# Kernel tuning notes

Measured on AMD Instinct MI355X. Metric: run time of the kernel, lower is better.

Reference implementation:

```python
import jax, jax.numpy as jnp
import numpy as np

ALPHA = 0.3      # keras LeakyReLU default
BN_EPS = 1e-3    # keras BatchNormalization default
RF, STRIDE = 8, 8


def leaky(x):
    return jnp.where(x >= 0, x, ALPHA * x)


def batchnorm(x, gamma, beta):
    # training-mode BN (train_flag=True): batch statistics over N,H,W
    mean = jnp.mean(x, axis=(0, 1, 2), keepdims=True)
    var = jnp.var(x, axis=(0, 1, 2), keepdims=True)
    return gamma * (x - mean) * jax.lax.rsqrt(var + BN_EPS) + beta


def cbl(x, W, gamma, beta):
    y = jax.lax.conv_general_dilated(x, W, (1, 1), 'SAME',
                                     dimension_numbers=('NHWC', 'HWIO', 'NHWC'))
    return leaky(batchnorm(y, gamma, beta))


def tcbl(x, W, gamma, beta):
    y = jax.lax.conv_transpose(x, W, (2, 2), 'SAME',
                               dimension_numbers=('NHWC', 'HWIO', 'NHWC'))
    return leaky(batchnorm(y, gamma, beta))


def setup_inputs() -> dict:
    key = jax.random.key(0)
    ks = jax.random.split(key, 8)
    B, H, W, C = 8, 128, 128, 128
    nH = (H - RF) // STRIDE + 1
    nW = (W - RF) // STRIDE + 1
    nWin = nH * nW  # 256
    inputs = jax.random.normal(ks[0], (B, H, W, C), dtype=jnp.float32)
    conv_scale = 1.0 / np.sqrt(3 * 3 * C)
    Wq = jax.random.normal(ks[1], (3, 3, C, 128), dtype=jnp.float32) * conv_scale
    Wk = jax.random.normal(ks[2], (3, 3, C, 128), dtype=jnp.float32) * conv_scale
    beta_bias = jax.random.normal(ks[3], (1, 1, 1, nWin), dtype=jnp.float32) * 0.05
    Wt = jax.random.normal(ks[4], (4, 4, nWin, 128), dtype=jnp.float32) / np.sqrt(4 * 4 * nWin)
    return {
        'inputs': inputs,
        'Wq': Wq, 'gq': jnp.ones((128,), jnp.float32), 'bq': jnp.zeros((128,), jnp.float32),
        'Wk': Wk, 'gk': jnp.ones((128,), jnp.float32), 'bk': jnp.zeros((128,), jnp.float32),
        'beta_bias': beta_bias,
        'g1': jnp.ones((nWin,), jnp.float32), 'b1': jnp.zeros((nWin,), jnp.float32),
        'Wt': Wt, 'gt': jnp.ones((128,), jnp.float32), 'bt': jnp.zeros((128,), jnp.float32),
    }


def reference(inputs, Wq, gq, bq, Wk, gk, bk, beta_bias, g1, b1, Wt, gt, bt):
    Q = cbl(inputs, Wq, gq, bq)   # (B,H,W,C)
    K = cbl(inputs, Wk, gk, bk)
    B, H, W, C = Q.shape
    nH = (H - RF) // STRIDE + 1
    nW = (W - RF) // STRIDE + 1
    # window start indices -> (n, RF) gather index grids
    hh = (jnp.arange(nH) * STRIDE)[:, None] + jnp.arange(RF)[None, :]
    ww = (jnp.arange(nW) * STRIDE)[:, None] + jnp.arange(RF)[None, :]

    def patches(x):
        # (B, nH, nW, RF, RF, C) -> (B, nWin, RF*RF*C)
        p = x[:, hh[:, None, :, None], ww[None, :, None, :], :]
        return p.reshape(B, nH * nW, RF * RF * C)

    Qp = patches(Q)
    Kp = patches(K)
    # sim[b, f, q] = <K window f, Q window q>; collapses the 4-nested loop
    sim = jnp.einsum('bfd,bqd->bfq', Kp, Qp).reshape(B, nH, nW, nH * nW)
    sim = sim + beta_bias
    act = leaky(batchnorm(sim, g1, b1))
    return tcbl(act, Wt, gt, bt)  # (B, 2*nH, 2*nW, 128)
```

## Files before the change

### kernel.cpp

```cpp
#include <hip/hip_runtime.h>

typedef __attribute__((ext_vector_type(8))) short bf16x8;
typedef __attribute__((ext_vector_type(8))) unsigned short u16x8;
typedef __attribute__((ext_vector_type(4))) float f32x4;

__device__ __forceinline__ unsigned short f2b(float x) {
    unsigned int u = __float_as_uint(x);
    u += 0x7FFFu + ((u >> 16) & 1u);
    return (unsigned short)(u >> 16);
}
__device__ __forceinline__ float b2f(unsigned short h) {
    return __uint_as_float(((unsigned int)h) << 16);
}
__device__ __forceinline__ float lrelu(float v) { return v >= 0.f ? v : 0.3f * v; }

#define GLL(gp, lp) __builtin_amdgcn_global_load_lds( \
    (const __attribute__((address_space(1))) unsigned int*)(gp), \
    (__attribute__((address_space(3))) unsigned int*)(lp), 16, 0, 0)


__global__ __launch_bounds__(256) void k0a_prep(
        const float* __restrict__ Wq, const float* __restrict__ Wk,
        const float* __restrict__ Wt, unsigned short* __restrict__ WqT,
        unsigned short* __restrict__ WkT, unsigned short* __restrict__ WtT,
        float* __restrict__ S) {
    int idx = blockIdx.x * 256 + threadIdx.x;
    int gs = gridDim.x * 256;
    for (int i = idx; i < 2048; i += gs) S[i] = 0.f;
    for (int i = idx; i < 147456; i += gs) {
        int tap = i >> 14, r = i & 16383, ci = r >> 7, co = r & 127;
        int ch = ci >> 6, e = ci & 63;
        int dst = ((tap * 2 + ch) * 128 + co) * 64 + (((e >> 3) ^ (co & 7)) << 3) + (e & 7);
        WqT[dst] = f2b(Wq[i]);
        WkT[dst] = f2b(Wk[i]);
    }
    for (int i = idx; i < 524288; i += gs) {
        int t = i >> 15, r = i & 32767, ci = r >> 7, co = r & 127;
        WtT[(((size_t)t << 7) + co) * 256 + ci] = f2b(Wt[i]);
    }
}

__global__ __launch_bounds__(256) void k0b_padx(const float* __restrict__ X,
                                                unsigned short* __restrict__ Xb) {
    int c = blockIdx.x * 256 + threadIdx.x;
    int k8 = c & 7;
    int t = c >> 3;
    int wp = t % 130; t /= 130;
    int ch = t & 1; t >>= 1;
    int hp = t % 130; int b = t / 130;
    u16x8 o;
    if (hp >= 1 && hp <= 128 && wp >= 1 && wp <= 128) {
        const float* s = X + (((size_t)(b * 128 + hp - 1) * 128) + (wp - 1)) * 128 + ch * 64 + k8 * 8;
        float4 f0 = *(const float4*)(s);
        float4 f1 = *(const float4*)(s + 4);
        o[0] = f2b(f0.x); o[1] = f2b(f0.y); o[2] = f2b(f0.z); o[3] = f2b(f0.w);
        o[4] = f2b(f1.x); o[5] = f2b(f1.y); o[6] = f2b(f1.z); o[7] = f2b(f1.w);
    } else {
#pragma unroll
        for (int j = 0; j < 8; ++j) o[j] = 0;
    }
    *(u16x8*)&Xb[(size_t)c * 8] = o;
}

__global__ __launch_bounds__(512, 4) void k1_conv(
        const unsigned short* __restrict__ Xb,
        const unsigned short* __restrict__ WqT, const unsigned short* __restrict__ WkT,
        unsigned short* __restrict__ Qraw, unsigned short* __restrict__ Kraw,
        float* __restrict__ S) {
    __shared__ unsigned short s_row[2 * 130 * 72];
    __shared__ unsigned short s_w[2][128 * 64];
    __shared__ float s_st[256];
    const int tid = threadIdx.x;
    const int x = blockIdx.x;
    const int conv = x & 1, hp = (x >> 1) & 63, b = x >> 7;
    const int h0 = hp * 2;
    const int lane = tid & 63, wv = tid >> 6;
    const int wm = wv & 3, wn = wv >> 2;
    const int l15 = lane & 15, kof = (lane >> 4) * 8;
    const int ar = wm >> 1;
    const int awb = (wm & 1) * 64;
    const int nb = wn * 64;

    const unsigned short* W = conv ? WkT : WqT;
    const int gofs = wv * 2048 + lane * 16;

    f32x4 acc[4][4];
#pragma unroll
    for (int i = 0; i < 4; ++i)
#pragma unroll
        for (int j = 0; j < 4; ++j) acc[i][j] = (f32x4){0.f, 0.f, 0.f, 0.f};
    if (tid < 256) s_st[tid] = 0.f;

    {
        const char* src = (const char*)W;
        char* dst = (char*)&s_w[0][0] + wv * 2048;
        GLL(src + gofs, dst);
        GLL(src + gofs + 1024, dst + 1024);
    }

#pragma unroll
    for (int ch = 0; ch < 2; ++ch) {
#pragma unroll
        for (int dy = 0; dy < 3; ++dy) {
#pragma unroll
            for (int dx = 0; dx < 3; ++dx) {
                const int p = (ch * 3 + dy) * 3 + dx;
                __builtin_amdgcn_s_barrier();
                if (dx == 0) {
                    const unsigned short* src0 = Xb + (size_t)((b * 130 + h0 + dy) * 2 + ch) * 8320;
                    const unsigned short* src1 = Xb + (size_t)((b * 130 + h0 + dy + 1) * 2 + ch) * 8320;
                    for (int c = tid; c < 2080; c += 512) {
                        int r = (c >= 1040);
                        int cw = r ? c - 1040 : c;
                        int w = cw >> 3, k8 = cw & 7;
                        *(u16x8*)&s_row[(r * 130 + w) * 72 + k8 * 8] =
                            *(const u16x8*)&((r ? src1 : src0)[cw * 8]);
                    }
                }
                if (p < 17) {
                    const int pn = p + 1;
                    const int nch = pn / 9, ntap = pn % 9;
                    const char* src = (const char*)(W + ((size_t)(ntap * 2 + nch) << 13));
                    char* dst = (char*)&s_w[pn & 1][0] + wv * 2048;
                    GLL(src + gofs, dst);
                    GLL(src + gofs + 1024, dst + 1024);
                    asm volatile("s_waitcnt vmcnt(2) lgkmcnt(0)" ::: "memory");
                } else {
                    asm volatile("s_waitcnt vmcnt(0) lgkmcnt(0)" ::: "memory");
                }
                __builtin_amdgcn_sched_barrier(0);
                __builtin_amdgcn_s_barrier();
                const unsigned short* wb = &s_w[p & 1][0];
#pragma unroll
                for (int kc = 0; kc < 2; ++kc) {
                    const int ci = kc * 32 + kof;
                    bf16x8 a[4], bb[4];
#pragma unroll
                    for (int mf = 0; mf < 4; ++mf)
                        a[mf] = *(const bf16x8*)&s_row[(ar * 130 + awb + mf * 16 + l15 + dx) * 72 + ci];
#pragma unroll
                    for (int nf = 0; nf < 4; ++nf) {
                        int co = nb + nf * 16 + l15;
                        bb[nf] = *(const bf16x8*)&wb[co * 64 + (((ci >> 3) ^ (co & 7)) << 3)];
                    }
#pragma unroll
                    for (int mf = 0; mf < 4; ++mf)
#pragma unroll
                        for (int nf = 0; nf < 4; ++nf)
                            acc[mf][nf] = __builtin_amdgcn_mfma_f32_16x16x32_bf16(
                                a[mf], bb[nf], acc[mf][nf], 0, 0, 0);
                }
            }
        }
    }
    __syncthreads();
    unsigned short* obase = conv ? Kraw : Qraw;
    const int h = h0 + ar;
    float sl[4] = {0.f, 0.f, 0.f, 0.f}, ssl[4] = {0.f, 0.f, 0.f, 0.f};
#pragma unroll
    for (int mf = 0; mf < 4; ++mf)
#pragma unroll
        for (int nf = 0; nf < 4; ++nf)
#pragma unroll
            for (int r = 0; r < 4; ++r) {
                float v = acc[mf][nf][r];
                int w = awb + mf * 16 + (lane >> 4) * 4 + r;
                int co = nb + nf * 16 + l15;
                obase[((size_t)(b * 128 + h) * 128 + w) * 128 + co] = f2b(v);
                sl[nf] += v; ssl[nf] += v * v;
            }
#pragma unroll
    for (int nf = 0; nf < 4; ++nf) {
        float s = sl[nf], ss = ssl[nf];
        s += __shfl_xor(s, 16); s += __shfl_xor(s, 32);
        ss += __shfl_xor(ss, 16); ss += __shfl_xor(ss, 32);
        if (lane < 16) {
            int chn = nb + nf * 16 + lane;
            atomicAdd(&s_st[chn], s);
            atomicAdd(&s_st[128 + chn], ss);
        }
    }
    __syncthreads();
    if (tid < 256) {
        int dst = (tid < 128) ? (conv * 128 + tid) : (256 + conv * 128 + (tid - 128));
        atomicAdd(&S[dst], s_st[tid]);
    }
}

__global__ void k2a_fin(const float* __restrict__ gq, const float* __restrict__ bq,
                        const float* __restrict__ gk, const float* __restrict__ bk,
                        const float* __restrict__ S, float* __restrict__ P) {
    int c = threadIdx.x;
    const float inv_n = 1.f / 131072.f;
    float mean = S[c] * inv_n;
    float var = S[256 + c] * inv_n - mean * mean;
    float g  = (c < 128) ? gq[c] : gk[c - 128];
    float be = (c < 128) ? bq[c] : bk[c - 128];
    float sc = g * rsqrtf(var + 1e-3f);
    P[c] = sc;
    P[256 + c] = be - mean * sc;
}

__global__ __launch_bounds__(512, 2) void k3_sim(const unsigned short* __restrict__ Qp,
                                                 const unsigned short* __restrict__ Kp,
                                                 const float* __restrict__ P,
                                                 float* __restrict__ part) {
    __shared__ unsigned short sA[128 * 136];
    __shared__ unsigned short sB[128 * 136];
    const int tid = threadIdx.x;
    const int x = blockIdx.x;
    const int kc = x & 15, ni = (x >> 4) & 1, mi = (x >> 5) & 1, b = x >> 6;
    const int lane = tid & 63, wv = tid >> 6;
    const int wm = wv & 1, wn = wv >> 1;
    f32x4 acc[4][2];
#pragma unroll
    for (int i = 0; i < 4; ++i)
#pragma unroll
        for (int j = 0; j < 2; ++j) acc[i][j] = (f32x4){0.f, 0.f, 0.f, 0.f};
    const int kof = (lane >> 4) * 8;
    const int arow = wm * 64 + (lane & 15);
    const int brow = wn * 32 + (lane & 15);

    for (int s = 0; s < 4; ++s) {
        const int p = kc * 4 + s, py = p >> 3, px = p & 7;
        __syncthreads();
        for (int c = tid; c < 2048; c += 512) {
            int r = c >> 4, k8 = c & 15;
            int cb = k8 * 8;
            int f = mi * 128 + r;
            size_t sa = ((size_t)(b * 128 + ((f >> 4) * 8 + py)) * 128 + ((f & 15) * 8 + px)) * 128 + cb;
            int q = ni * 128 + r;
            size_t sb = ((size_t)(b * 128 + ((q >> 4) * 8 + py)) * 128 + ((q & 15) * 8 + px)) * 128 + cb;
            u16x8 va = *(const u16x8*)&Kp[sa];
            u16x8 vb = *(const u16x8*)&Qp[sb];
            u16x8 oa, ob;
#pragma unroll
            for (int j = 0; j < 8; ++j) {
                float fk = b2f(va[j]);
                fk = lrelu(P[128 + cb + j] * fk + P[384 + cb + j]);
                oa[j] = f2b(fk);
                float fq = b2f(vb[j]);
                fq = lrelu(P[cb + j] * fq + P[256 + cb + j]);
                ob[j] = f2b(fq);
            }
            *(u16x8*)&sA[r * 136 + cb] = oa;
            *(u16x8*)&sB[r * 136 + cb] = ob;
        }
        __syncthreads();
#pragma unroll
        for (int k4 = 0; k4 < 4; ++k4) {
            const int ci = k4 * 32 + kof;
            bf16x8 a[4], bb[2];
#pragma unroll
            for (int mf = 0; mf < 4; ++mf)
                a[mf] = *(const bf16x8*)&sA[(arow + mf * 16) * 136 + ci];
#pragma unroll
            for (int nf = 0; nf < 2; ++nf)
                bb[nf] = *(const bf16x8*)&sB[(brow + nf * 16) * 136 + ci];
#pragma unroll
            for (int mf = 0; mf < 4; ++mf)
#pragma unroll
                for (int nf = 0; nf < 2; ++nf)
                    acc[mf][nf] = __builtin_amdgcn_mfma_f32_16x16x32_bf16(
                        a[mf], bb[nf], acc[mf][nf], 0, 0, 0);
        }
    }
    const size_t base = (size_t)(kc * 8 + b) * 65536;
#pragma unroll
    for (int mf = 0; mf < 4; ++mf)
#pragma unroll
        for (int nf = 0; nf < 2; ++nf)
#pragma unroll
            for (int r = 0; r < 4; ++r) {
                int f = mi * 128 + wm * 64 + mf * 16 + (lane >> 4) * 4 + r;
                int q = ni * 128 + wn * 32 + nf * 16 + (lane & 15);
                part[base + (size_t)f * 256 + q] = acc[mf][nf][r];
            }
}

__global__ __launch_bounds__(256) void k4_red(const float* __restrict__ part,
                                              const float* __restrict__ beta,
                                              float* __restrict__ sim, float* __restrict__ S) {
    int row0 = blockIdx.x * 8;
    int q = threadIdx.x;
    float bsum = 0.f, bss = 0.f;
    float bb = beta[q];
    for (int rr = 0; rr < 8; ++rr) {
        int row = row0 + rr;
        float s = 0.f;
#pragma unroll
        for (int kcc = 0; kcc < 16; ++kcc)
            s += part[(size_t)kcc * 524288 + (size_t)row * 256 + q];
        s += bb;
        sim[(size_t)row * 256 + q] = s;
        bsum += s; bss += s * s;
    }
    atomicAdd(&S[512 + q], bsum);
    atomicAdd(&S[768 + q], bss);
}

__global__ void k5a_fin(const float* __restrict__ g1, const float* __restrict__ b1,
                        const float* __restrict__ S, float* __restrict__ P) {
    int c = threadIdx.x;
    const float inv_n = 1.f / 2048.f;
    float mean = S[512 + c] * inv_n;
    float var = S[768 + c] * inv_n - mean * mean;
    float sc = g1[c] * rsqrtf(var + 1e-3f);
    P[512 + c] = sc;
    P[768 + c] = b1[c] - mean * sc;
}

__global__ __launch_bounds__(256) void k5b_act(const float* __restrict__ sim,
                                               const float* __restrict__ P,
                                               unsigned short* __restrict__ actp) {
    int c = blockIdx.x * 256 + threadIdx.x;
    int k8 = c & 31;
    int t = c >> 5;
    int jp = t % 18; t /= 18;
    int ip = t % 18; int b = t / 18;
    u16x8 o;
    if (ip >= 1 && ip <= 16 && jp >= 1 && jp <= 16) {
        int f = (ip - 1) * 16 + (jp - 1);
        const float* s = sim + (size_t)(b * 256 + f) * 256 + k8 * 8;
#pragma unroll
        for (int j = 0; j < 8; ++j) {
            int ci = k8 * 8 + j;
            o[j] = f2b(lrelu(P[512 + ci] * s[j] + P[768 + ci]));
        }
    } else {
#pragma unroll
        for (int j = 0; j < 8; ++j) o[j] = 0;
    }
    *(u16x8*)&actp[(size_t)c * 8] = o;
}

__global__ __launch_bounds__(512, 2) void k6_tconv(const unsigned short* __restrict__ actp,
                                                   const unsigned short* __restrict__ WtT,
                                                   float* __restrict__ y, float* __restrict__ S) {
    __shared__ unsigned short sA[64 * 264];
    __shared__ unsigned short sB[128 * 264];
    const int tid = threadIdx.x;
    const int x = blockIdx.x;
    const int iq = x & 3, pw = (x >> 2) & 1, ph = (x >> 3) & 1, b = x >> 4;
    const int lane = tid & 63, wv = tid >> 6;
    f32x4 acc[4];
#pragma unroll
    for (int i = 0; i < 4; ++i) acc[i] = (f32x4){0.f, 0.f, 0.f, 0.f};
    const int kof = (lane >> 4) * 8;
    const int arow = lane & 15;
    const int bco = wv * 16 + (lane & 15);

    for (int a2 = 0; a2 < 2; ++a2)
        for (int c2 = 0; c2 < 2; ++c2) {
            const int kh = ph + 2 * a2, kw = pw + 2 * c2;
            __syncthreads();
            for (int c = tid; c < 2048; c += 512) {
                int r = c >> 5, k8 = c & 31;
                int i = iq * 4 + (r >> 4), j = r & 15;
                size_t sa = (size_t)((b * 18 + (i + a2 + ph)) * 18 + (j + c2 + pw)) * 256 + k8 * 8;
                *(u16x8*)&sA[r * 264 + k8 * 8] = *(const u16x8*)&actp[sa];
            }
            for (int c = tid; c < 4096; c += 512) {
                int co = c >> 5, k8 = c & 31;
                size_t sb = (size_t)((kh * 4 + kw) * 128 + co) * 256 + k8 * 8;
                *(u16x8*)&sB[co * 264 + k8 * 8] = *(const u16x8*)&WtT[sb];
            }
            __syncthreads();
#pragma unroll
            for (int k8c = 0; k8c < 8; ++k8c) {
                const int ci = k8c * 32 + kof;
                bf16x8 bb = *(const bf16x8*)&sB[bco * 264 + ci];
#pragma unroll
                for (int mf = 0; mf < 4; ++mf) {
                    bf16x8 a = *(const bf16x8*)&sA[(arow + mf * 16) * 264 + ci];
                    acc[mf] = __builtin_amdgcn_mfma_f32_16x16x32_bf16(a, bb, acc[mf], 0, 0, 0);
                }
            }
        }
    float sl = 0.f, ssl = 0.f;
#pragma unroll
    for (int mf = 0; mf < 4; ++mf)
#pragma unroll
        for (int r = 0; r < 4; ++r) {
            float v = acc[mf][r];
            int m = mf * 16 + (lane >> 4) * 4 + r;
            int i = iq * 4 + (m >> 4), j = m & 15;
            int oh = 2 * i + ph, ow = 2 * j + pw;
            y[(size_t)((b * 32 + oh) * 32 + ow) * 128 + bco] = v;
            sl += v; ssl += v * v;
        }
    sl += __shfl_xor(sl, 16); sl += __shfl_xor(sl, 32);
    ssl += __shfl_xor(ssl, 16); ssl += __shfl_xor(ssl, 32);
    if (lane < 16) {
        atomicAdd(&S[1024 + wv * 16 + lane], sl);
        atomicAdd(&S[1152 + wv * 16 + lane], ssl);
    }
}

__global__ void k7_fin(const float* __restrict__ gt, const float* __restrict__ bt,
                       const float* __restrict__ S, float* __restrict__ P) {
    int c = threadIdx.x;
    const float inv_n = 1.f / 8192.f;
    float mean = S[1024 + c] * inv_n;
    float var = S[1152 + c] * inv_n - mean * mean;
    float sc = gt[c] * rsqrtf(var + 1e-3f);
    P[1024 + c] = sc;
    P[1280 + c] = bt[c] - mean * sc;
}

__global__ __launch_bounds__(256) void k8_out(const float* __restrict__ y,
                                              const float* __restrict__ P,
                                              float* __restrict__ out) {
    int c = blockIdx.x * 256 + threadIdx.x;
    const float4 v = *(const float4*)&y[(size_t)c * 4];
    int cb = (c & 31) * 4;
    float4 o;
    o.x = lrelu(P[1024 + cb + 0] * v.x + P[1280 + cb + 0]);
    o.y = lrelu(P[1024 + cb + 1] * v.y + P[1280 + cb + 1]);
    o.z = lrelu(P[1024 + cb + 2] * v.z + P[1280 + cb + 2]);
    o.w = lrelu(P[1024 + cb + 3] * v.w + P[1280 + cb + 3]);
    *(float4*)&out[(size_t)c * 4] = o;
}

extern "C" void kernel_launch(void* const* d_in, const int* in_sizes, int n_in,
                              void* d_out, int out_size, void* d_ws, size_t ws_size,
                              hipStream_t stream) {
    (void)in_sizes; (void)n_in; (void)out_size; (void)ws_size;
    const float* X    = (const float*)d_in[0];
    const float* Wq   = (const float*)d_in[1];
    const float* gq   = (const float*)d_in[2];
    const float* bq   = (const float*)d_in[3];
    const float* Wk   = (const float*)d_in[4];
    const float* gk   = (const float*)d_in[5];
    const float* bk   = (const float*)d_in[6];
    const float* beta = (const float*)d_in[7];
    const float* g1   = (const float*)d_in[8];
    const float* b1   = (const float*)d_in[9];
    const float* Wt   = (const float*)d_in[10];
    const float* gt   = (const float*)d_in[11];
    const float* bt   = (const float*)d_in[12];

    char* ws = (char*)d_ws;
    unsigned short* Qraw = (unsigned short*)(ws + 0ull);
    unsigned short* Kraw = (unsigned short*)(ws + 33554432ull);
    unsigned short* WqT  = (unsigned short*)(ws + 67108864ull);
    unsigned short* WkT  = (unsigned short*)(ws + 67403776ull);
    unsigned short* WtT  = (unsigned short*)(ws + 67698688ull);
    float* S             = (float*)(ws + 68747264ull);
    float* P             = (float*)(ws + 68755456ull);
    unsigned short* Xb   = (unsigned short*)(ws + 70858752ull);
    float* part          = (float*)(ws + 70858752ull);
    float* sim           = (float*)(ws + 0ull);
    unsigned short* actp = (unsigned short*)(ws + 4194304ull);
    float* y             = (float*)(ws + 8388608ull);
    float* out           = (float*)d_out;

    k0a_prep<<<1024, 256, 0, stream>>>(Wq, Wk, Wt, WqT, WkT, WtT, S);
    k0b_padx<<<8450, 256, 0, stream>>>(X, Xb);
    k1_conv<<<1024, 512, 0, stream>>>(Xb, WqT, WkT, Qraw, Kraw, S);
    k2a_fin<<<1, 256, 0, stream>>>(gq, bq, gk, bk, S, P);
    k3_sim<<<512, 512, 0, stream>>>(Qraw, Kraw, P, part);
    k4_red<<<256, 256, 0, stream>>>(part, beta, sim, S);
    k5a_fin<<<1, 256, 0, stream>>>(g1, b1, S, P);
    k5b_act<<<729, 256, 0, stream>>>(sim, P, actp);
    k6_tconv<<<128, 512, 0, stream>>>(actp, WtT, y, S);
    k7_fin<<<1, 128, 0, stream>>>(gt, bt, S, P);
    k8_out<<<1024, 256, 0, stream>>>(y, P, out);
}
```

Measured before the change: 178.5 us.

## Pipeline conv input rows via async LDS loads and fold BN finalize kernels into consumers

The padded input is relaid out as four 32-channel slabs with a lane-swizzled 136-wide row, so the conv kernel can stream input rows into double-buffered LDS with global_load_lds. Those row loads are prefetched one stage ahead alongside the weight tiles, instead of being copied synchronously through registers. The three single-block BN finalize kernels are removed and their scale/shift math is recomputed per block inside the consuming kernels, which cuts launches at the cost of redundant tiny work. MFMA sections are also wrapped in s_setprio.

```diff
diff --git a/kernel.cpp b/kernel.cpp
--- a/kernel.cpp
+++ b/kernel.cpp
@@ -29,8 +29,8 @@
     for (int i = idx; i < 2048; i += gs) S[i] = 0.f;
     for (int i = idx; i < 147456; i += gs) {
         int tap = i >> 14, r = i & 16383, ci = r >> 7, co = r & 127;
-        int ch = ci >> 6, e = ci & 63;
-        int dst = ((tap * 2 + ch) * 128 + co) * 64 + (((e >> 3) ^ (co & 7)) << 3) + (e & 7);
+        int q = ci >> 5, cl = (ci >> 3) & 3, e = ci & 7;
+        int dst = (((tap * 4 + q) * 128 + co) * 4 + (cl ^ (co & 3))) * 8 + e;
         WqT[dst] = f2b(Wq[i]);
         WkT[dst] = f2b(Wk[i]);
     }
@@ -43,14 +43,16 @@
 __global__ __launch_bounds__(256) void k0b_padx(const float* __restrict__ X,
                                                 unsigned short* __restrict__ Xb) {
     int c = blockIdx.x * 256 + threadIdx.x;
-    int k8 = c & 7;
-    int t = c >> 3;
-    int wp = t % 130; t /= 130;
-    int ch = t & 1; t >>= 1;
-    int hp = t % 130; int b = t / 130;
+    if (c >= 2263040) return;
+    int pc = c & 3;
+    int t = c >> 2;
+    int w = t % 136; t /= 136;
+    int h = t % 130; t /= 130;
+    int q = t & 3; int b = t >> 2;
     u16x8 o;
-    if (hp >= 1 && hp <= 128 && wp >= 1 && wp <= 128) {
-        const float* s = X + (((size_t)(b * 128 + hp - 1) * 128) + (wp - 1)) * 128 + ch * 64 + k8 * 8;
+    if (h >= 1 && h <= 128 && w >= 1 && w <= 128) {
+        int ci = q * 32 + ((pc ^ (w & 3)) << 3);
+        const float* s = X + (((size_t)(b * 128 + h - 1) * 128) + (w - 1)) * 128 + ci;
         float4 f0 = *(const float4*)(s);
         float4 f1 = *(const float4*)(s + 4);
         o[0] = f2b(f0.x); o[1] = f2b(f0.y); o[2] = f2b(f0.z); o[3] = f2b(f0.w);
@@ -67,8 +69,8 @@
         const unsigned short* __restrict__ WqT, const unsigned short* __restrict__ WkT,
         unsigned short* __restrict__ Qraw, unsigned short* __restrict__ Kraw,
         float* __restrict__ S) {
-    __shared__ unsigned short s_row[2 * 130 * 72];
-    __shared__ unsigned short s_w[2][128 * 64];
+    __shared__ unsigned short s_row[2][8704];
+    __shared__ unsigned short s_w[2][4096];
     __shared__ float s_st[256];
     const int tid = threadIdx.x;
     const int x = blockIdx.x;
@@ -76,13 +78,13 @@
     const int h0 = hp * 2;
     const int lane = tid & 63, wv = tid >> 6;
     const int wm = wv & 3, wn = wv >> 2;
-    const int l15 = lane & 15, kof = (lane >> 4) * 8;
+    const int l15 = lane & 15;
+    const int cl = lane >> 4;
     const int ar = wm >> 1;
     const int awb = (wm & 1) * 64;
     const int nb = wn * 64;
-
     const unsigned short* W = conv ? WkT : WqT;
-    const int gofs = wv * 2048 + lane * 16;
+    const size_t xbb = (size_t)b * 2263040;
 
     f32x4 acc[4][4];
 #pragma unroll
@@ -92,66 +94,54 @@
     if (tid < 256) s_st[tid] = 0.f;
 
     {
-        const char* src = (const char*)W;
-        char* dst = (char*)&s_w[0][0] + wv * 2048;
-        GLL(src + gofs, dst);
-        GLL(src + gofs + 1024, dst + 1024);
-    }
-
-#pragma unroll
-    for (int ch = 0; ch < 2; ++ch) {
-#pragma unroll
-        for (int dy = 0; dy < 3; ++dy) {
-#pragma unroll
-            for (int dx = 0; dx < 3; ++dx) {
-                const int p = (ch * 3 + dy) * 3 + dx;
-                __builtin_amdgcn_s_barrier();
-                if (dx == 0) {
-                    const unsigned short* src0 = Xb + (size_t)((b * 130 + h0 + dy) * 2 + ch) * 8320;
-                    const unsigned short* src1 = Xb + (size_t)((b * 130 + h0 + dy + 1) * 2 + ch) * 8320;
-                    for (int c = tid; c < 2080; c += 512) {
-                        int r = (c >= 1040);
-                        int cw = r ? c - 1040 : c;
-                        int w = cw >> 3, k8 = cw & 7;
-                        *(u16x8*)&s_row[(r * 130 + w) * 72 + k8 * 8] =
-                            *(const u16x8*)&((r ? src1 : src0)[cw * 8]);
-                    }
-                }
-                if (p < 17) {
-                    const int pn = p + 1;
-                    const int nch = pn / 9, ntap = pn % 9;
-                    const char* src = (const char*)(W + ((size_t)(ntap * 2 + nch) << 13));
-                    char* dst = (char*)&s_w[pn & 1][0] + wv * 2048;
-                    GLL(src + gofs, dst);
-                    GLL(src + gofs + 1024, dst + 1024);
-                    asm volatile("s_waitcnt vmcnt(2) lgkmcnt(0)" ::: "memory");
-                } else {
-                    asm volatile("s_waitcnt vmcnt(0) lgkmcnt(0)" ::: "memory");
-                }
-                __builtin_amdgcn_sched_barrier(0);
-                __builtin_amdgcn_s_barrier();
-                const unsigned short* wb = &s_w[p & 1][0];
-#pragma unroll
-                for (int kc = 0; kc < 2; ++kc) {
-                    const int ci = kc * 32 + kof;
-                    bf16x8 a[4], bb[4];
-#pragma unroll
-                    for (int mf = 0; mf < 4; ++mf)
-                        a[mf] = *(const bf16x8*)&s_row[(ar * 130 + awb + mf * 16 + l15 + dx) * 72 + ci];
-#pragma unroll
-                    for (int nf = 0; nf < 4; ++nf) {
-                        int co = nb + nf * 16 + l15;
-                        bb[nf] = *(const bf16x8*)&wb[co * 64 + (((ci >> 3) ^ (co & 7)) << 3)];
-                    }
-#pragma unroll
-                    for (int mf = 0; mf < 4; ++mf)
-#pragma unroll
-                        for (int nf = 0; nf < 4; ++nf)
-                            acc[mf][nf] = __builtin_amdgcn_mfma_f32_16x16x32_bf16(
-                                a[mf], bb[nf], acc[mf][nf], 0, 0, 0);
-                }
-            }
-        }
+        GLL((const char*)W + wv * 1024 + lane * 16, (char*)&s_w[0][0] + wv * 1024);
+        const char* rsrc = (const char*)(Xb + xbb + (size_t)h0 * 4352);
+        for (int u = wv; u < 17; u += 8)
+            GLL(rsrc + u * 1024 + lane * 16, (char*)&s_row[0][0] + u * 1024);
+    }
+
+#pragma unroll
+    for (int p = 0; p < 36; ++p) {
+        const int s = p / 3, dx = p % 3;
+        __builtin_amdgcn_s_barrier();
+        if (p < 35) {
+            const int pn = p + 1, ntap = pn % 9, nq = pn / 9;
+            const char* wsrc = (const char*)(W + (size_t)(ntap * 4 + nq) * 4096);
+            GLL(wsrc + wv * 1024 + lane * 16, (char*)&s_w[pn & 1][0] + wv * 1024);
+        }
+        if (dx == 0 && s < 11) {
+            const int sn = s + 1, nq2 = sn / 3, ndy = sn % 3;
+            const char* rsrc = (const char*)(Xb + xbb + (size_t)(nq2 * 130 + h0 + ndy) * 4352);
+            char* rdst = (char*)&s_row[sn & 1][0];
+            for (int u = wv; u < 17; u += 8)
+                GLL(rsrc + u * 1024 + lane * 16, rdst + u * 1024);
+        }
+        if (p == 35)                  asm volatile("s_waitcnt vmcnt(0)" ::: "memory");
+        else if (dx == 2 || s == 11)  asm volatile("s_waitcnt vmcnt(1)" ::: "memory");
+        else                          asm volatile("s_waitcnt vmcnt(3)" ::: "memory");
+        __builtin_amdgcn_sched_barrier(0);
+        __builtin_amdgcn_s_barrier();
+        const unsigned short* wb = &s_w[p & 1][0];
+        const unsigned short* rb = &s_row[s & 1][0];
+        bf16x8 a[4], bb[4];
+#pragma unroll
+        for (int mf = 0; mf < 4; ++mf) {
+            int wph = awb + mf * 16 + l15 + dx;
+            a[mf] = *(const bf16x8*)&rb[(ar * 136 + wph) * 32 + ((cl ^ (wph & 3)) << 3)];
+        }
+#pragma unroll
+        for (int nf = 0; nf < 4; ++nf) {
+            int co = nb + nf * 16 + l15;
+            bb[nf] = *(const bf16x8*)&wb[co * 32 + ((cl ^ (co & 3)) << 3)];
+        }
+        __builtin_amdgcn_s_setprio(1);
+#pragma unroll
+        for (int mf = 0; mf < 4; ++mf)
+#pragma unroll
+            for (int nf = 0; nf < 4; ++nf)
+                acc[mf][nf] = __builtin_amdgcn_mfma_f32_16x16x32_bf16(
+                    a[mf], bb[nf], acc[mf][nf], 0, 0, 0);
+        __builtin_amdgcn_s_setprio(0);
     }
     __syncthreads();
     unsigned short* obase = conv ? Kraw : Qraw;
@@ -187,31 +177,30 @@
     }
 }
 
-__global__ void k2a_fin(const float* __restrict__ gq, const float* __restrict__ bq,
-                        const float* __restrict__ gk, const float* __restrict__ bk,
-                        const float* __restrict__ S, float* __restrict__ P) {
-    int c = threadIdx.x;
-    const float inv_n = 1.f / 131072.f;
-    float mean = S[c] * inv_n;
-    float var = S[256 + c] * inv_n - mean * mean;
-    float g  = (c < 128) ? gq[c] : gk[c - 128];
-    float be = (c < 128) ? bq[c] : bk[c - 128];
-    float sc = g * rsqrtf(var + 1e-3f);
-    P[c] = sc;
-    P[256 + c] = be - mean * sc;
-}
-
 __global__ __launch_bounds__(512, 2) void k3_sim(const unsigned short* __restrict__ Qp,
                                                  const unsigned short* __restrict__ Kp,
-                                                 const float* __restrict__ P,
+                                                 const float* __restrict__ S,
+                                                 const float* __restrict__ gq, const float* __restrict__ bq,
+                                                 const float* __restrict__ gk, const float* __restrict__ bk,
                                                  float* __restrict__ part) {
     __shared__ unsigned short sA[128 * 136];
     __shared__ unsigned short sB[128 * 136];
+    __shared__ float s_p[512];
     const int tid = threadIdx.x;
     const int x = blockIdx.x;
     const int kc = x & 15, ni = (x >> 4) & 1, mi = (x >> 5) & 1, b = x >> 6;
     const int lane = tid & 63, wv = tid >> 6;
     const int wm = wv & 1, wn = wv >> 1;
+    if (tid < 256) {
+        const float inv_n = 1.f / 131072.f;
+        float mean = S[tid] * inv_n;
+        float var = S[256 + tid] * inv_n - mean * mean;
+        float g  = (tid < 128) ? gq[tid] : gk[tid - 128];
+        float be = (tid < 128) ? bq[tid] : bk[tid - 128];
+        float sc = g * rsqrtf(var + 1e-3f);
+        s_p[tid] = sc;
+        s_p[256 + tid] = be - mean * sc;
+    }
     f32x4 acc[4][2];
 #pragma unroll
     for (int i = 0; i < 4; ++i)
@@ -237,10 +226,10 @@
 #pragma unroll
             for (int j = 0; j < 8; ++j) {
                 float fk = b2f(va[j]);
-                fk = lrelu(P[128 + cb + j] * fk + P[384 + cb + j]);
+                fk = lrelu(s_p[128 + cb + j] * fk + s_p[384 + cb + j]);
                 oa[j] = f2b(fk);
                 float fq = b2f(vb[j]);
-                fq = lrelu(P[cb + j] * fq + P[256 + cb + j]);
+                fq = lrelu(s_p[cb + j] * fq + s_p[256 + cb + j]);
                 ob[j] = f2b(fq);
             }
             *(u16x8*)&sA[r * 136 + cb] = oa;
@@ -299,21 +288,23 @@
     atomicAdd(&S[768 + q], bss);
 }
 
-__global__ void k5a_fin(const float* __restrict__ g1, const float* __restrict__ b1,
-                        const float* __restrict__ S, float* __restrict__ P) {
-    int c = threadIdx.x;
-    const float inv_n = 1.f / 2048.f;
-    float mean = S[512 + c] * inv_n;
-    float var = S[768 + c] * inv_n - mean * mean;
-    float sc = g1[c] * rsqrtf(var + 1e-3f);
-    P[512 + c] = sc;
-    P[768 + c] = b1[c] - mean * sc;
-}
-
 __global__ __launch_bounds__(256) void k5b_act(const float* __restrict__ sim,
-                                               const float* __restrict__ P,
+                                               const float* __restrict__ S,
+                                               const float* __restrict__ g1, const float* __restrict__ b1,
                                                unsigned short* __restrict__ actp) {
+    __shared__ float s_p[512];
+    {
+        int c = threadIdx.x;
+        const float inv_n = 1.f / 2048.f;
+        float mean = S[512 + c] * inv_n;
+        float var = S[768 + c] * inv_n - mean * mean;
+        float sc = g1[c] * rsqrtf(var + 1e-3f);
+        s_p[c] = sc;
+        s_p[256 + c] = b1[c] - mean * sc;
+    }
+    __syncthreads();
     int c = blockIdx.x * 256 + threadIdx.x;
+    if (c >= 186624) return;
     int k8 = c & 31;
     int t = c >> 5;
     int jp = t % 18; t /= 18;
@@ -325,7 +316,7 @@
 #pragma unroll
         for (int j = 0; j < 8; ++j) {
             int ci = k8 * 8 + j;
-            o[j] = f2b(lrelu(P[512 + ci] * s[j] + P[768 + ci]));
+            o[j] = f2b(lrelu(s_p[ci] * s[j] + s_p[256 + ci]));
         }
     } else {
 #pragma unroll
@@ -397,28 +388,29 @@
     }
 }
 
-__global__ void k7_fin(const float* __restrict__ gt, const float* __restrict__ bt,
-                       const float* __restrict__ S, float* __restrict__ P) {
-    int c = threadIdx.x;
-    const float inv_n = 1.f / 8192.f;
-    float mean = S[1024 + c] * inv_n;
-    float var = S[1152 + c] * inv_n - mean * mean;
-    float sc = gt[c] * rsqrtf(var + 1e-3f);
-    P[1024 + c] = sc;
-    P[1280 + c] = bt[c] - mean * sc;
-}
-
 __global__ __launch_bounds__(256) void k8_out(const float* __restrict__ y,
-                                              const float* __restrict__ P,
+                                              const float* __restrict__ S,
+                                              const float* __restrict__ gt, const float* __restrict__ bt,
                                               float* __restrict__ out) {
+    __shared__ float s_p[256];
+    if (threadIdx.x < 128) {
+        int c = threadIdx.x;
+        const float inv_n = 1.f / 8192.f;
+        float mean = S[1024 + c] * inv_n;
+        float var = S[1152 + c] * inv_n - mean * mean;
+        float sc = gt[c] * rsqrtf(var + 1e-3f);
+        s_p[c] = sc;
+        s_p[128 + c] = bt[c] - mean * sc;
+    }
+    __syncthreads();
     int c = blockIdx.x * 256 + threadIdx.x;
     const float4 v = *(const float4*)&y[(size_t)c * 4];
     int cb = (c & 31) * 4;
     float4 o;
-    o.x = lrelu(P[1024 + cb + 0] * v.x + P[1280 + cb + 0]);
-    o.y = lrelu(P[1024 + cb + 1] * v.y + P[1280 + cb + 1]);
-    o.z = lrelu(P[1024 + cb + 2] * v.z + P[1280 + cb + 2]);
-    o.w = lrelu(P[1024 + cb + 3] * v.w + P[1280 + cb + 3]);
+    o.x = lrelu(s_p[cb + 0] * v.x + s_p[128 + cb + 0]);
+    o.y = lrelu(s_p[cb + 1] * v.y + s_p[128 + cb + 1]);
+    o.z = lrelu(s_p[cb + 2] * v.z + s_p[128 + cb + 2]);
+    o.w = lrelu(s_p[cb + 3] * v.w + s_p[128 + cb + 3]);
     *(float4*)&out[(size_t)c * 4] = o;
 }
 
@@ -447,23 +439,19 @@
     unsigned short* WkT  = (unsigned short*)(ws + 67403776ull);
     unsigned short* WtT  = (unsigned short*)(ws + 67698688ull);
     float* S             = (float*)(ws + 68747264ull);
-    float* P             = (float*)(ws + 68755456ull);
-    unsigned short* Xb   = (unsigned short*)(ws + 70858752ull);
-    float* part          = (float*)(ws + 70858752ull);
+    unsigned short* Xb   = (unsigned short*)(ws + 68761600ull);
+    float* part          = (float*)(ws + 68761600ull);
     float* sim           = (float*)(ws + 0ull);
     unsigned short* actp = (unsigned short*)(ws + 4194304ull);
     float* y             = (float*)(ws + 8388608ull);
     float* out           = (float*)d_out;
 
     k0a_prep<<<1024, 256, 0, stream>>>(Wq, Wk, Wt, WqT, WkT, WtT, S);
-    k0b_padx<<<8450, 256, 0, stream>>>(X, Xb);
+    k0b_padx<<<8840, 256, 0, stream>>>(X, Xb);
     k1_conv<<<1024, 512, 0, stream>>>(Xb, WqT, WkT, Qraw, Kraw, S);
-    k2a_fin<<<1, 256, 0, stream>>>(gq, bq, gk, bk, S, P);
-    k3_sim<<<512, 512, 0, stream>>>(Qraw, Kraw, P, part);
+    k3_sim<<<512, 512, 0, stream>>>(Qraw, Kraw, S, gq, bq, gk, bk, part);
     k4_red<<<256, 256, 0, stream>>>(part, beta, sim, S);
-    k5a_fin<<<1, 256, 0, stream>>>(g1, b1, S, P);
-    k5b_act<<<729, 256, 0, stream>>>(sim, P, actp);
+    k5b_act<<<729, 256, 0, stream>>>(sim, S, g1, b1, actp);
     k6_tconv<<<128, 512, 0, stream>>>(actp, WtT, y, S);
-    k7_fin<<<1, 128, 0, stream>>>(gt, bt, S, P);
-    k8_out<<<1024, 256, 0, stream>>>(y, P, out);
-}
+    k8_out<<<1024, 256, 0, stream>>>(y, S, gt, bt, out);
+}
```

New measurement: 200.5 us. 12.3% more time.
